# Kernel tuning notes

Measured on AMD Instinct MI355X. Metric: run time of the kernel, lower is better.

The kernel has to match this reference:

```python
import jax, jax.numpy as jnp
import numpy as np
import math

B, S, D = 1, 4096, 1024
H, DK = 16, 64
WINDOW = 256
GLOBAL = 16


def setup_inputs() -> dict:
    key = jax.random.key(0)
    ks = jax.random.split(key, 8)
    scale = 1.0 / math.sqrt(D)  # xavier-ish scale for projections
    return {
        "query": jax.random.normal(ks[0], (B, S, D), jnp.float32),
        "key": jax.random.normal(ks[1], (B, S, D), jnp.float32),
        "value": jax.random.normal(ks[2], (B, S, D), jnp.float32),
        "Wq": jax.random.normal(ks[3], (D, D), jnp.float32) * scale,
        "bq": jnp.zeros((D,), jnp.float32),
        "Wk": jax.random.normal(ks[4], (D, D), jnp.float32) * scale,
        "bk": jnp.zeros((D,), jnp.float32),
        "Wv": jax.random.normal(ks[5], (D, D), jnp.float32) * scale,
        "bv": jnp.zeros((D,), jnp.float32),
        "Wo": jax.random.normal(ks[6], (D, D), jnp.float32) * scale,
        "bo": jnp.zeros((D,), jnp.float32),
    }


def _split_heads(x):
    # [B, S, D] -> [B, H, S, DK]
    return x.reshape(B, S, H, DK).transpose(0, 2, 1, 3)


def reference(query, key, value, Wq, bq, Wk, bk, Wv, bv, Wo, bo):
    Q = _split_heads(query @ Wq + bq)   # [B,H,S,DK]
    K = _split_heads(key @ Wk + bk)
    V = _split_heads(value @ Wv + bv)

    scores = jnp.einsum("bhqd,bhkd->bhqk", Q, K) / math.sqrt(DK)  # [B,H,S,S]

    i = jnp.arange(S)[:, None]
    j = jnp.arange(S)[None, :]
    local = jnp.abs(i - j) <= WINDOW
    glob = (i < GLOBAL) | (j < GLOBAL)
    causal = j <= i
    mask = (local | glob) & causal  # [S,S]

    scores = jnp.where(mask[None, None], scores, -jnp.inf)
    probs = jax.nn.softmax(scores, axis=-1)  # dropout is identity (p=0 / eval)

    out = jnp.einsum("bhqk,bhkd->bhqd", probs, V)  # [B,H,S,DK]
    out = out.transpose(0, 2, 1, 3).reshape(B, S, D)
    return out @ Wo + bo
```

## Files before the change

kernel.cpp:

```cpp
#include <hip/hip_runtime.h>

typedef __bf16 bf16_t;
typedef __attribute__((ext_vector_type(8))) __bf16 bf16x8;
typedef __attribute__((ext_vector_type(4))) __bf16 bf16x4;
typedef __attribute__((ext_vector_type(2))) __bf16 bf16x2;
typedef __attribute__((ext_vector_type(4))) float f32x4;

#define S_LEN 4096
#define D_MODEL 1024
#define NH 16
#define DKH 64
#define WIN 256
#define NGLOB 16
#define HSZ (S_LEN * DKH)

__device__ inline void g2l16(const void* g, void* l) {
  __builtin_amdgcn_global_load_lds(
      (__attribute__((address_space(1))) void*)(void*)g,
      (__attribute__((address_space(3))) void*)l, 16, 0, 0);
}

template <bool AF32>
__device__ __forceinline__ void gemm_pipe(const void* __restrict__ Ap,
                                          const bf16_t* __restrict__ Bt,
                                          int m0, int n0, int wave, int lane,
                                          bf16_t* As, bf16_t* Bs,
                                          f32x4 acc[4][4]) {
  const float* Af = (const float*)Ap;
  const bf16_t* Ah = (const bf16_t*)Ap;
  const int wr = wave >> 1, wc = wave & 1;
#pragma unroll
  for (int i = 0; i < 4; i++)
#pragma unroll
    for (int j = 0; j < 4; j++) acc[i][j] = {0.f, 0.f, 0.f, 0.f};

  const int arow_l = lane >> 2;
  const int aslot = lane & 3;
  const int ssl = (lane & 7) ^ (lane >> 3);
  const int srowB = 2 * (lane >> 3) + (ssl >> 2);
  const int scolB = 8 * (ssl & 3);
  const int fr = lane & 15;
  const int fkg = lane >> 4;

#define A_LDS_OFF(c)                                                       \
  ((((c)*16 + arow_l) >> 1) * 64 +                                         \
   (((((c)*16 + arow_l) & 1) << 2 | aslot) ^ ((((c)*16 + arow_l) >> 1) & 7)) * 8)

#pragma unroll
  for (int i = 0; i < 2; i++) {
    const int c = wave * 2 + i;
    const int r = c * 16 + arow_l;
    if constexpr (AF32) {
      const float* s = Af + (size_t)(m0 + r) * D_MODEL + aslot * 8;
      const float4 x = *(const float4*)s;
      const float4 y = *(const float4*)(s + 4);
      bf16x8 w = {(bf16_t)x.x, (bf16_t)x.y, (bf16_t)x.z, (bf16_t)x.w,
                  (bf16_t)y.x, (bf16_t)y.y, (bf16_t)y.z, (bf16_t)y.w};
      *(bf16x8*)&As[A_LDS_OFF(c)] = w;
    } else {
      *(bf16x8*)&As[A_LDS_OFF(c)] =
          *(const bf16x8*)(Ah + (size_t)(m0 + r) * D_MODEL + aslot * 8);
    }
    g2l16(Bt + (size_t)(n0 + c * 16 + srowB) * D_MODEL + scolB, &Bs[c * 512]);
  }
  __syncthreads();

#pragma unroll 2
  for (int t = 0; t < 32; ++t) {
    const int buf = t & 1;
    const bool hn = (t < 31);
    float4 ax0{}, ay0{}, ax1{}, ay1{};
    bf16x8 ah0{}, ah1{};
    if (hn) {
      const int kn = (t + 1) * 32;
      {
        const int r0 = (wave * 2) * 16 + arow_l;
        const int r1 = (wave * 2 + 1) * 16 + arow_l;
        if constexpr (AF32) {
          const float* s0 = Af + (size_t)(m0 + r0) * D_MODEL + kn + aslot * 8;
          const float* s1 = Af + (size_t)(m0 + r1) * D_MODEL + kn + aslot * 8;
          ax0 = *(const float4*)s0;
          ay0 = *(const float4*)(s0 + 4);
          ax1 = *(const float4*)s1;
          ay1 = *(const float4*)(s1 + 4);
        } else {
          ah0 = *(const bf16x8*)(Ah + (size_t)(m0 + r0) * D_MODEL + kn + aslot * 8);
          ah1 = *(const bf16x8*)(Ah + (size_t)(m0 + r1) * D_MODEL + kn + aslot * 8);
        }
        g2l16(Bt + (size_t)(n0 + (wave * 2) * 16 + srowB) * D_MODEL + kn + scolB,
              &Bs[(buf ^ 1) * 4096 + (wave * 2) * 512]);
        g2l16(Bt + (size_t)(n0 + (wave * 2 + 1) * 16 + srowB) * D_MODEL + kn + scolB,
              &Bs[(buf ^ 1) * 4096 + (wave * 2 + 1) * 512]);
      }
    }
    __builtin_amdgcn_sched_barrier(0);
    bf16x8 af[4], bfr[4];
#pragma unroll
    for (int m = 0; m < 4; m++) {
      const int rr = wr * 64 + m * 16 + fr;
      af[m] = *(const bf16x8*)&As[buf * 4096 + (rr >> 1) * 64 +
                                  ((((rr & 1) << 2) + fkg) ^ ((rr >> 1) & 7)) * 8];
    }
#pragma unroll
    for (int n = 0; n < 4; n++) {
      const int rr = wc * 64 + n * 16 + fr;
      bfr[n] = *(const bf16x8*)&Bs[buf * 4096 + (rr >> 1) * 64 +
                                   ((((rr & 1) << 2) + fkg) ^ ((rr >> 1) & 7)) * 8];
    }
#pragma unroll
    for (int m = 0; m < 4; m++)
#pragma unroll
      for (int n = 0; n < 4; n++)
        acc[m][n] = __builtin_amdgcn_mfma_f32_16x16x32_bf16(af[m], bfr[n],
                                                            acc[m][n], 0, 0, 0);
    __builtin_amdgcn_sched_barrier(0);
    if (hn) {
      bf16x8 w0, w1;
      if constexpr (AF32) {
        w0 = bf16x8{(bf16_t)ax0.x, (bf16_t)ax0.y, (bf16_t)ax0.z, (bf16_t)ax0.w,
                    (bf16_t)ay0.x, (bf16_t)ay0.y, (bf16_t)ay0.z, (bf16_t)ay0.w};
        w1 = bf16x8{(bf16_t)ax1.x, (bf16_t)ax1.y, (bf16_t)ax1.z, (bf16_t)ax1.w,
                    (bf16_t)ay1.x, (bf16_t)ay1.y, (bf16_t)ay1.z, (bf16_t)ay1.w};
      } else {
        w0 = ah0;
        w1 = ah1;
      }
      *(bf16x8*)&As[(buf ^ 1) * 4096 + A_LDS_OFF(wave * 2)] = w0;
      *(bf16x8*)&As[(buf ^ 1) * 4096 + A_LDS_OFF(wave * 2 + 1)] = w1;
    }
    __syncthreads();
  }
#undef A_LDS_OFF
}

__global__ __launch_bounds__(256, 3) void gemm_qkv(
    const float* __restrict__ Xq, const float* __restrict__ Xk,
    const float* __restrict__ Xv, const bf16_t* __restrict__ Wt,
    const float* __restrict__ bq, const float* __restrict__ bk,
    const float* __restrict__ bv, bf16_t* __restrict__ Qo,
    bf16_t* __restrict__ Ko, bf16_t* __restrict__ Vto) {
  __shared__ bf16_t As[2 * 128 * 32];
  __shared__ bf16_t Bs[2 * 128 * 32];
  const int lin = blockIdx.x;
  const int wg = ((lin & 7) * 96) + (lin >> 3);
  const int n0 = (wg & 7) * 128;
  const int m0 = ((wg >> 3) & 31) * 128;
  const int which = wg >> 8;

  const float* A = which == 0 ? Xq : which == 1 ? Xk : Xv;
  const bf16_t* Bt = Wt + (size_t)which * (D_MODEL * D_MODEL);
  const float* bias = which == 0 ? bq : which == 1 ? bk : bv;

  const int wave = threadIdx.x >> 6, lane = threadIdx.x & 63;
  f32x4 acc[4][4];
  gemm_pipe<true>(A, Bt, m0, n0, wave, lane, As, Bs, acc);

  const int wr = wave >> 1, wc = wave & 1;
  const int cr = (lane >> 4) * 4;
  const int cc = lane & 15;
#pragma unroll
  for (int m = 0; m < 4; m++) {
    const int rowg = m0 + wr * 64 + m * 16 + cr;
#pragma unroll
    for (int n = 0; n < 4; n++) {
      const int colg = n0 + wc * 64 + n * 16 + cc;
      const float bv_ = bias[colg];
      const int h = colg >> 6, d = colg & 63;
#pragma unroll
      for (int r = 0; r < 4; r++) {
        const int s = rowg + r;
        const float v = acc[m][n][r] + bv_;
        if (which == 0)
          Qo[h * HSZ + s * DKH + d] = (bf16_t)(v * 0.125f);
        else if (which == 1)
          Ko[h * HSZ + s * DKH + d] = (bf16_t)v;
        else
          Vto[h * HSZ + d * S_LEN + s] = (bf16_t)v;
      }
    }
  }
}

__global__ __launch_bounds__(256, 3) void gemm_out(
    const bf16_t* __restrict__ A_, const bf16_t* __restrict__ Bt_,
    const float* __restrict__ bias, float* __restrict__ Cout) {
  __shared__ bf16_t As[2 * 128 * 32];
  __shared__ bf16_t Bs[2 * 128 * 32];
  const int lin = blockIdx.x;
  const int wg = ((lin & 7) * 32) + (lin >> 3);
  const int n0 = (wg & 7) * 128;
  const int m0 = (wg >> 3) * 128;
  const int wave = threadIdx.x >> 6, lane = threadIdx.x & 63;
  f32x4 acc[4][4];
  gemm_pipe<false>(A_, Bt_, m0, n0, wave, lane, As, Bs, acc);

  const int wr = wave >> 1, wc = wave & 1;
  const int cr = (lane >> 4) * 4;
  const int cc = lane & 15;
#pragma unroll
  for (int m = 0; m < 4; m++) {
    const int rowg = m0 + wr * 64 + m * 16 + cr;
#pragma unroll
    for (int n = 0; n < 4; n++) {
      const int colg = n0 + wc * 64 + n * 16 + cc;
      const float bv_ = bias[colg];
#pragma unroll
      for (int r = 0; r < 4; r++)
        Cout[(size_t)(rowg + r) * D_MODEL + colg] = acc[m][n][r] + bv_;
    }
  }
}

__global__ void convw(const float* __restrict__ W0, const float* __restrict__ W1,
                      const float* __restrict__ W2, const float* __restrict__ W3,
                      bf16_t* __restrict__ out) {
  __shared__ float t[64][65];
  const float* W = blockIdx.z == 0 ? W0 : blockIdx.z == 1 ? W1
                  : blockIdx.z == 2 ? W2 : W3;
  bf16_t* Wt = out + (size_t)blockIdx.z * (D_MODEL * D_MODEL);
  const int k0 = blockIdx.y * 64, n0 = blockIdx.x * 64;
  const int tx = threadIdx.x & 63, ty = threadIdx.x >> 6;
#pragma unroll
  for (int i = 0; i < 16; i++) {
    const int r = i * 4 + ty;
    t[r][tx] = W[(size_t)(k0 + r) * D_MODEL + n0 + tx];
  }
  __syncthreads();
#pragma unroll
  for (int i = 0; i < 16; i++) {
    const int r = i * 4 + ty;
    Wt[(size_t)(n0 + r) * D_MODEL + k0 + tx] = (bf16_t)t[tx][r];
  }
}

__global__ __launch_bounds__(256) void attn_kern(const bf16_t* __restrict__ Q,
                                                 const bf16_t* __restrict__ K,
                                                 const bf16_t* __restrict__ V,
                                                 bf16_t* __restrict__ O) {
  __shared__ bf16_t p_lds[4][16 * 40];
  const int wave = threadIdx.x >> 6, lane = threadIdx.x & 63;
  const int h = blockIdx.y;
  const int q0 = blockIdx.x * 64 + wave * 16;
  const bf16_t* Qh = Q + h * HSZ;
  const bf16_t* Kh = K + h * HSZ;
  const bf16_t* Vh = V + h * HSZ;

  const int fr = lane & 15;
  const int fk = (lane >> 4) * 8;
  const int cr = (lane >> 4) * 4;

  const bf16x8 aq0 = *(const bf16x8*)&Qh[(q0 + fr) * DKH + fk];
  const bf16x8 aq1 = *(const bf16x8*)&Qh[(q0 + fr) * DKH + 32 + fk];

  f32x4 acc_o[4];
#pragma unroll
  for (int i = 0; i < 4; i++) acc_o[i] = {0.f, 0.f, 0.f, 0.f};
  float m_run = -1e30f, l_run = 0.f;

  const int kt_end = (q0 + 15) >> 5;
  int kt_lo = (q0 - WIN) >> 5;
  if (kt_lo < 0) kt_lo = 0;
  const int nt = kt_end - kt_lo + 1 + (kt_lo > 0 ? 1 : 0);

#define TILE_KB(t) ((kt_lo > 0) ? ((t) == 0 ? 0 : (kt_lo + (t)-1) * 32) : (t)*32)
#define LOADK(kb, A0, A1, A2, A3)                              \
  A0 = *(const bf16x8*)&Kh[((kb) + fr) * DKH + fk];            \
  A1 = *(const bf16x8*)&Kh[((kb) + fr) * DKH + 32 + fk];       \
  A2 = *(const bf16x8*)&Kh[((kb) + 16 + fr) * DKH + fk];       \
  A3 = *(const bf16x8*)&Kh[((kb) + 16 + fr) * DKH + 32 + fk];

  bf16x8 kc0, kc1, kc2, kc3;
  {
    const int kb0 = TILE_KB(0);
    LOADK(kb0, kc0, kc1, kc2, kc3)
  }

  const int iq = q0 + fr;
  bf16_t* prow = &p_lds[wave][fr * 40];
  const bf16x8* pread = (const bf16x8*)&p_lds[wave][fr * 40 + fk];

  for (int t = 0; t < nt; t++) {
    const int kb = TILE_KB(t);
    bf16x8 kn0, kn1, kn2, kn3;
    const bool have_next = (t + 1 < nt);
    if (have_next) {
      const int nkb = TILE_KB(t + 1);
      LOADK(nkb, kn0, kn1, kn2, kn3)
    }
    bf16x8 vf0 = *(const bf16x8*)&Vh[(0 * 16 + fr) * S_LEN + kb + fk];
    bf16x8 vf1 = *(const bf16x8*)&Vh[(1 * 16 + fr) * S_LEN + kb + fk];
    bf16x8 vf2 = *(const bf16x8*)&Vh[(2 * 16 + fr) * S_LEN + kb + fk];
    bf16x8 vf3 = *(const bf16x8*)&Vh[(3 * 16 + fr) * S_LEN + kb + fk];

    f32x4 s0 = {0.f, 0.f, 0.f, 0.f}, s1 = {0.f, 0.f, 0.f, 0.f};
    s0 = __builtin_amdgcn_mfma_f32_16x16x32_bf16(kc0, aq0, s0, 0, 0, 0);
    s0 = __builtin_amdgcn_mfma_f32_16x16x32_bf16(kc1, aq1, s0, 0, 0, 0);
    s1 = __builtin_amdgcn_mfma_f32_16x16x32_bf16(kc2, aq0, s1, 0, 0, 0);
    s1 = __builtin_amdgcn_mfma_f32_16x16x32_bf16(kc3, aq1, s1, 0, 0, 0);

    float v[8];
#pragma unroll
    for (int r = 0; r < 4; r++) {
      const int j0 = kb + cr + r, j1 = j0 + 16;
      v[r] = (j0 <= iq && (iq - j0 <= WIN || j0 < NGLOB)) ? s0[r] : -1e30f;
      v[4 + r] = (j1 <= iq && (iq - j1 <= WIN || j1 < NGLOB)) ? s1[r] : -1e30f;
    }
    float mt = fmaxf(fmaxf(fmaxf(v[0], v[1]), fmaxf(v[2], v[3])),
                     fmaxf(fmaxf(v[4], v[5]), fmaxf(v[6], v[7])));
    mt = fmaxf(mt, __shfl_xor(mt, 16));
    mt = fmaxf(mt, __shfl_xor(mt, 32));
    const float mn = fmaxf(m_run, mt);
    const float alpha = __expf(m_run - mn);
    m_run = mn;
    float p[8];
    float ps = 0.f;
#pragma unroll
    for (int i = 0; i < 8; i++) {
      p[i] = __expf(v[i] - mn);
      ps += p[i];
    }
    ps += __shfl_xor(ps, 16);
    ps += __shfl_xor(ps, 32);
    l_run = l_run * alpha + ps;

    *(bf16x2*)&prow[cr] = bf16x2{(bf16_t)p[0], (bf16_t)p[1]};
    *(bf16x2*)&prow[cr + 2] = bf16x2{(bf16_t)p[2], (bf16_t)p[3]};
    *(bf16x2*)&prow[16 + cr] = bf16x2{(bf16_t)p[4], (bf16_t)p[5]};
    *(bf16x2*)&prow[16 + cr + 2] = bf16x2{(bf16_t)p[6], (bf16_t)p[7]};

    float alpha_r[4];
#pragma unroll
    for (int r = 0; r < 4; r++) alpha_r[r] = __shfl(alpha, cr + r);

    asm volatile("" ::: "memory");
    const bf16x8 pa = *pread;
    asm volatile("" ::: "memory");

#pragma unroll
    for (int fd = 0; fd < 4; fd++) {
#pragma unroll
      for (int r = 0; r < 4; r++) acc_o[fd][r] *= alpha_r[r];
    }
    acc_o[0] = __builtin_amdgcn_mfma_f32_16x16x32_bf16(pa, vf0, acc_o[0], 0, 0, 0);
    acc_o[1] = __builtin_amdgcn_mfma_f32_16x16x32_bf16(pa, vf1, acc_o[1], 0, 0, 0);
    acc_o[2] = __builtin_amdgcn_mfma_f32_16x16x32_bf16(pa, vf2, acc_o[2], 0, 0, 0);
    acc_o[3] = __builtin_amdgcn_mfma_f32_16x16x32_bf16(pa, vf3, acc_o[3], 0, 0, 0);

    if (have_next) {
      kc0 = kn0; kc1 = kn1; kc2 = kn2; kc3 = kn3;
    }
  }

  const float linv = 1.0f / l_run;
  float inv_r[4];
#pragma unroll
  for (int r = 0; r < 4; r++) inv_r[r] = __shfl(linv, cr + r);

#pragma unroll
  for (int fd = 0; fd < 4; fd++)
#pragma unroll
    for (int r = 0; r < 4; r++) {
      const int s = q0 + cr + r;
      O[(size_t)s * D_MODEL + h * DKH + fd * 16 + fr] =
          (bf16_t)(acc_o[fd][r] * inv_r[r]);
    }
}

extern "C" void kernel_launch(void* const* d_in, const int* in_sizes, int n_in,
                              void* d_out, int out_size, void* d_ws,
                              size_t ws_size, hipStream_t stream) {
  const float* query = (const float*)d_in[0];
  const float* key = (const float*)d_in[1];
  const float* value = (const float*)d_in[2];
  const float* Wq = (const float*)d_in[3];
  const float* bq = (const float*)d_in[4];
  const float* Wk = (const float*)d_in[5];
  const float* bk = (const float*)d_in[6];
  const float* Wv = (const float*)d_in[7];
  const float* bv = (const float*)d_in[8];
  const float* Wo = (const float*)d_in[9];
  const float* bo = (const float*)d_in[10];

  char* ws = (char*)d_ws;
  bf16_t* Qb = (bf16_t*)(ws);
  bf16_t* Kb = (bf16_t*)(ws + (8ull << 20));
  bf16_t* Vtb = (bf16_t*)(ws + (16ull << 20));
  bf16_t* Wt = (bf16_t*)(ws + (24ull << 20));
  bf16_t* Ab = (bf16_t*)(ws + (32ull << 20));

  const size_t WSTRIDE = (size_t)D_MODEL * D_MODEL;

  convw<<<dim3(16, 16, 4), 256, 0, stream>>>(Wq, Wk, Wv, Wo, Wt);

  gemm_qkv<<<768, 256, 0, stream>>>(query, key, value, Wt, bq, bk, bv, Qb, Kb,
                                    Vtb);

  attn_kern<<<dim3(64, 16), 256, 0, stream>>>(Qb, Kb, Vtb, Ab);

  gemm_out<<<256, 256, 0, stream>>>(Ab, Wt + 3 * WSTRIDE, bo, (float*)d_out);
}
```

Before: 129.1 us.

## Replace double-buffered GEMM pipeline with single-buffer direct-to-LDS fp32 A loads

Drops the register-prefetch double-buffered k-loop in both GEMMs and uses one LDS buffer that is loaded and then computed in each k-step, separated by barriers. For the QKV projection, fp32 activations now go straight into LDS through global_load_lds and are converted to bf16 when fragments are read, not converted in registers before staging. The launch-bounds occupancy hint is also removed. This cuts register pressure and VGPR round-trips, but global loads no longer overlap with MFMA work, and the fp32 A tile doubles the LDS traffic for A.

```diff
diff --git a/kernel.cpp b/kernel.cpp
--- a/kernel.cpp
+++ b/kernel.cpp
@@ -21,11 +21,13 @@
 }
 
 template <bool AF32>
-__device__ __forceinline__ void gemm_pipe(const void* __restrict__ Ap,
+__device__ __forceinline__ void gemm_body(const void* __restrict__ Ap,
                                           const bf16_t* __restrict__ Bt,
                                           int m0, int n0, int wave, int lane,
-                                          bf16_t* As, bf16_t* Bs,
+                                          char* AsRaw, bf16_t* Bs,
                                           f32x4 acc[4][4]) {
+  float* Asf = (float*)AsRaw;
+  bf16_t* Ash = (bf16_t*)AsRaw;
   const float* Af = (const float*)Ap;
   const bf16_t* Ah = (const bf16_t*)Ap;
   const int wr = wave >> 1, wc = wave & 1;
@@ -34,78 +36,62 @@
 #pragma unroll
     for (int j = 0; j < 4; j++) acc[i][j] = {0.f, 0.f, 0.f, 0.f};
 
-  const int arow_l = lane >> 2;
-  const int aslot = lane & 3;
   const int ssl = (lane & 7) ^ (lane >> 3);
   const int srowB = 2 * (lane >> 3) + (ssl >> 2);
   const int scolB = 8 * (ssl & 3);
+  const int arowF = lane >> 3;
+  const int aslotF = (lane & 7) ^ arowF;
   const int fr = lane & 15;
   const int fkg = lane >> 4;
 
-#define A_LDS_OFF(c)                                                       \
-  ((((c)*16 + arow_l) >> 1) * 64 +                                         \
-   (((((c)*16 + arow_l) & 1) << 2 | aslot) ^ ((((c)*16 + arow_l) >> 1) & 7)) * 8)
-
-#pragma unroll
-  for (int i = 0; i < 2; i++) {
-    const int c = wave * 2 + i;
-    const int r = c * 16 + arow_l;
+  for (int k0 = 0; k0 < D_MODEL; k0 += 32) {
     if constexpr (AF32) {
-      const float* s = Af + (size_t)(m0 + r) * D_MODEL + aslot * 8;
-      const float4 x = *(const float4*)s;
-      const float4 y = *(const float4*)(s + 4);
-      bf16x8 w = {(bf16_t)x.x, (bf16_t)x.y, (bf16_t)x.z, (bf16_t)x.w,
-                  (bf16_t)y.x, (bf16_t)y.y, (bf16_t)y.z, (bf16_t)y.w};
-      *(bf16x8*)&As[A_LDS_OFF(c)] = w;
+#pragma unroll
+      for (int i = 0; i < 4; i++) {
+        const int c = wave * 4 + i;
+        g2l16(Af + (size_t)(m0 + c * 8 + arowF) * D_MODEL + k0 + aslotF * 4,
+              &Asf[c * 256]);
+      }
     } else {
-      *(bf16x8*)&As[A_LDS_OFF(c)] =
-          *(const bf16x8*)(Ah + (size_t)(m0 + r) * D_MODEL + aslot * 8);
-    }
-    g2l16(Bt + (size_t)(n0 + c * 16 + srowB) * D_MODEL + scolB, &Bs[c * 512]);
-  }
-  __syncthreads();
-
-#pragma unroll 2
-  for (int t = 0; t < 32; ++t) {
-    const int buf = t & 1;
-    const bool hn = (t < 31);
-    float4 ax0{}, ay0{}, ax1{}, ay1{};
-    bf16x8 ah0{}, ah1{};
-    if (hn) {
-      const int kn = (t + 1) * 32;
-      {
-        const int r0 = (wave * 2) * 16 + arow_l;
-        const int r1 = (wave * 2 + 1) * 16 + arow_l;
-        if constexpr (AF32) {
-          const float* s0 = Af + (size_t)(m0 + r0) * D_MODEL + kn + aslot * 8;
-          const float* s1 = Af + (size_t)(m0 + r1) * D_MODEL + kn + aslot * 8;
-          ax0 = *(const float4*)s0;
-          ay0 = *(const float4*)(s0 + 4);
-          ax1 = *(const float4*)s1;
-          ay1 = *(const float4*)(s1 + 4);
-        } else {
-          ah0 = *(const bf16x8*)(Ah + (size_t)(m0 + r0) * D_MODEL + kn + aslot * 8);
-          ah1 = *(const bf16x8*)(Ah + (size_t)(m0 + r1) * D_MODEL + kn + aslot * 8);
-        }
-        g2l16(Bt + (size_t)(n0 + (wave * 2) * 16 + srowB) * D_MODEL + kn + scolB,
-              &Bs[(buf ^ 1) * 4096 + (wave * 2) * 512]);
-        g2l16(Bt + (size_t)(n0 + (wave * 2 + 1) * 16 + srowB) * D_MODEL + kn + scolB,
-              &Bs[(buf ^ 1) * 4096 + (wave * 2 + 1) * 512]);
+#pragma unroll
+      for (int i = 0; i < 2; i++) {
+        const int c = wave * 2 + i;
+        g2l16(Ah + (size_t)(m0 + c * 16 + srowB) * D_MODEL + k0 + scolB,
+              &Ash[c * 512]);
       }
     }
-    __builtin_amdgcn_sched_barrier(0);
+#pragma unroll
+    for (int i = 0; i < 2; i++) {
+      const int c = wave * 2 + i;
+      g2l16(Bt + (size_t)(n0 + c * 16 + srowB) * D_MODEL + k0 + scolB,
+            &Bs[c * 512]);
+    }
+    __syncthreads();
     bf16x8 af[4], bfr[4];
 #pragma unroll
     for (int m = 0; m < 4; m++) {
       const int rr = wr * 64 + m * 16 + fr;
-      af[m] = *(const bf16x8*)&As[buf * 4096 + (rr >> 1) * 64 +
-                                  ((((rr & 1) << 2) + fkg) ^ ((rr >> 1) & 7)) * 8];
+      if constexpr (AF32) {
+        const float4 x =
+            *(const float4*)&Asf[rr * 32 + (((fkg << 1) ^ (rr & 7)) << 2)];
+        const float4 y =
+            *(const float4*)&Asf[rr * 32 +
+                                 ((((fkg << 1) | 1) ^ (rr & 7)) << 2)];
+        af[m] = bf16x8{(bf16_t)x.x, (bf16_t)x.y, (bf16_t)x.z, (bf16_t)x.w,
+                       (bf16_t)y.x, (bf16_t)y.y, (bf16_t)y.z, (bf16_t)y.w};
+      } else {
+        af[m] = *(const bf16x8*)&Ash[(rr >> 1) * 64 +
+                                     ((((rr & 1) << 2) + fkg) ^
+                                      ((rr >> 1) & 7)) *
+                                         8];
+      }
     }
 #pragma unroll
     for (int n = 0; n < 4; n++) {
       const int rr = wc * 64 + n * 16 + fr;
-      bfr[n] = *(const bf16x8*)&Bs[buf * 4096 + (rr >> 1) * 64 +
-                                   ((((rr & 1) << 2) + fkg) ^ ((rr >> 1) & 7)) * 8];
+      bfr[n] = *(const bf16x8*)&Bs[(rr >> 1) * 64 +
+                                   ((((rr & 1) << 2) + fkg) ^ ((rr >> 1) & 7)) *
+                                       8];
     }
 #pragma unroll
     for (int m = 0; m < 4; m++)
@@ -113,34 +99,18 @@
       for (int n = 0; n < 4; n++)
         acc[m][n] = __builtin_amdgcn_mfma_f32_16x16x32_bf16(af[m], bfr[n],
                                                             acc[m][n], 0, 0, 0);
-    __builtin_amdgcn_sched_barrier(0);
-    if (hn) {
-      bf16x8 w0, w1;
-      if constexpr (AF32) {
-        w0 = bf16x8{(bf16_t)ax0.x, (bf16_t)ax0.y, (bf16_t)ax0.z, (bf16_t)ax0.w,
-                    (bf16_t)ay0.x, (bf16_t)ay0.y, (bf16_t)ay0.z, (bf16_t)ay0.w};
-        w1 = bf16x8{(bf16_t)ax1.x, (bf16_t)ax1.y, (bf16_t)ax1.z, (bf16_t)ax1.w,
-                    (bf16_t)ay1.x, (bf16_t)ay1.y, (bf16_t)ay1.z, (bf16_t)ay1.w};
-      } else {
-        w0 = ah0;
-        w1 = ah1;
-      }
-      *(bf16x8*)&As[(buf ^ 1) * 4096 + A_LDS_OFF(wave * 2)] = w0;
-      *(bf16x8*)&As[(buf ^ 1) * 4096 + A_LDS_OFF(wave * 2 + 1)] = w1;
-    }
     __syncthreads();
   }
-#undef A_LDS_OFF
-}
-
-__global__ __launch_bounds__(256, 3) void gemm_qkv(
+}
+
+__global__ __launch_bounds__(256) void gemm_qkv(
     const float* __restrict__ Xq, const float* __restrict__ Xk,
     const float* __restrict__ Xv, const bf16_t* __restrict__ Wt,
     const float* __restrict__ bq, const float* __restrict__ bk,
     const float* __restrict__ bv, bf16_t* __restrict__ Qo,
     bf16_t* __restrict__ Ko, bf16_t* __restrict__ Vto) {
-  __shared__ bf16_t As[2 * 128 * 32];
-  __shared__ bf16_t Bs[2 * 128 * 32];
+  __shared__ float Asf[128 * 32];
+  __shared__ bf16_t Bs[128 * 32];
   const int lin = blockIdx.x;
   const int wg = ((lin & 7) * 96) + (lin >> 3);
   const int n0 = (wg & 7) * 128;
@@ -153,7 +123,7 @@
 
   const int wave = threadIdx.x >> 6, lane = threadIdx.x & 63;
   f32x4 acc[4][4];
-  gemm_pipe<true>(A, Bt, m0, n0, wave, lane, As, Bs, acc);
+  gemm_body<true>(A, Bt, m0, n0, wave, lane, (char*)Asf, Bs, acc);
 
   const int wr = wave >> 1, wc = wave & 1;
   const int cr = (lane >> 4) * 4;
@@ -181,18 +151,19 @@
   }
 }
 
-__global__ __launch_bounds__(256, 3) void gemm_out(
-    const bf16_t* __restrict__ A_, const bf16_t* __restrict__ Bt_,
-    const float* __restrict__ bias, float* __restrict__ Cout) {
-  __shared__ bf16_t As[2 * 128 * 32];
-  __shared__ bf16_t Bs[2 * 128 * 32];
+__global__ __launch_bounds__(256) void gemm_out(const bf16_t* __restrict__ A_,
+                                                const bf16_t* __restrict__ Bt_,
+                                                const float* __restrict__ bias,
+                                                float* __restrict__ Cout) {
+  __shared__ bf16_t Ash[128 * 32];
+  __shared__ bf16_t Bs[128 * 32];
   const int lin = blockIdx.x;
   const int wg = ((lin & 7) * 32) + (lin >> 3);
   const int n0 = (wg & 7) * 128;
   const int m0 = (wg >> 3) * 128;
   const int wave = threadIdx.x >> 6, lane = threadIdx.x & 63;
   f32x4 acc[4][4];
-  gemm_pipe<false>(A_, Bt_, m0, n0, wave, lane, As, Bs, acc);
+  gemm_body<false>(A_, Bt_, m0, n0, wave, lane, (char*)Ash, Bs, acc);
 
   const int wr = wave >> 1, wc = wave & 1;
   const int cr = (lane >> 4) * 4;
```

After: 130.4 us. About the same (+1.0%).
